# Optimization experiments

Measured on AMD Instinct MI355X. Metric: run time of the kernel, lower is better.

The kernel has to match this reference:

```python
import jax, jax.numpy as jnp
import numpy as np
import itertools

SEQ, NF, K, SD, NB, NC, NOBJ = 8, 4, 3, 256, 512, 174, 10
BELTA, SUB, BATCH = 0.1, 10, 256
SCALES = list(range(NF, 0, -1))  # [4, 3, 2, 1]
D = (K + 1) * SD                 # per-frame fused feature dim = 1024


def _adjust_scales(seq_ind, is_test):
    # mirrors adjust_scale_train / adjust_scale_test
    scale_max = NF * 2
    if seq_ind < scale_max:
        return SCALES[-seq_ind:] if is_test else SCALES[-min(SUB, seq_ind):]
    return SCALES[:min(SUB, seq_ind) + 1]


def _plan(is_test):
    # Static (non-traced) relation-index plan: for each seq_ind, the set of
    # arithmetic-progression frame combinations selected by select_idx().
    plan = []
    for seq_ind in range(1, SEQ + 1):
        entries = []
        for scale in _adjust_scales(seq_ind, is_test):
            k = min(scale, seq_ind)
            division = seq_ind // scale
            sel = [r for r in itertools.combinations(range(seq_ind), k)
                   if np.all(np.diff(np.asarray(r)) == division)]
            if sel:
                entries.append((scale, np.asarray(sel, dtype=np.int32)))
        plan.append(entries)
    return plan


def _temporal_variation(init_input):
    # VLAD-style soft residuals. Source runs kmeans (non-deterministic,
    # numpy/detached); we use deterministic centers = first K points per clip
    # and reproduce the exact downstream math, including the (buggy but
    # faithful) scalar spectral-norm soft assignment shared by all points.
    x = init_input.reshape(-1, SEQ, NOBJ, SD)              # (B, S, O, d)
    flat = x.reshape(x.shape[0], SEQ * NOBJ, SD)           # (B, N, d)
    centers = flat[:, :K, :]                               # (B, K, d)
    diff = flat[:, None, :, :] - centers[:, :, None, :]    # (B, K, N, d)
    sig = jnp.linalg.svd(diff, compute_uv=False)[..., 0]   # matrix 2-norm per (b, k)
    w = jax.nn.softmax(-BELTA * sig ** 2, axis=-1)         # (B, K), same for every point
    # S[b,t,k,:] = sum_o w[b,k] * (x[b,t,o,:] - c[b,k,:])
    var = w[:, None, :, None] * (x.sum(axis=2)[:, :, None, :] - NOBJ * centers[:, None, :, :])
    return jax.lax.stop_gradient(var)  # source detaches via .detach().numpy()


def _fusion(x, w1, b1, w2, b2):
    # Sequential(ReLU, Linear, ReLU, Linear)
    h = jnp.maximum(jax.nn.relu(x) @ w1 + b1, 0.0)
    return h @ w2 + b2


def _forward(graph_out, init_input, params, is_test):
    B = graph_out.shape[0]
    var = _temporal_variation(init_input)                      # (B, S, K, d)
    new_input = jnp.concatenate([var.reshape(B, SEQ, K * SD), graph_out], axis=2)  # (B, S, D)
    rows = []
    for entries in _plan(bool(is_test)):
        acc = jnp.zeros((B, NC), graph_out.dtype)
        for scale, rel in entries:
            # batched gather of all sampled relations at once: (B, R, scale, D)
            g = new_input[:, rel, :].reshape(B, rel.shape[0], scale * D)
            acc = acc + _fusion(g, *params[scale]).sum(axis=1)
        rows.append(acc)
    return jnp.stack(rows, axis=1).reshape(B * SEQ, NC)


def setup_inputs():
    key = jax.random.key(0)
    ks = jax.random.split(key, 2 + 2 * len(SCALES))
    inp = {
        "graph_out": jax.random.normal(ks[0], (BATCH, SEQ, SD), jnp.float32),
        "init_input": jax.random.normal(ks[1], (BATCH * SEQ, NOBJ, SD), jnp.float32),
        "is_test": 0,
    }
    for i, s in enumerate(SCALES):
        inp[f"w1_{s}"] = jax.random.normal(ks[2 + 2 * i], (s * D, NB), jnp.float32) * 0.02
        inp[f"b1_{s}"] = jnp.zeros((NB,), jnp.float32)
        inp[f"w2_{s}"] = jax.random.normal(ks[3 + 2 * i], (NB, NC), jnp.float32) * 0.02
        inp[f"b2_{s}"] = jnp.zeros((NC,), jnp.float32)
    return inp


def reference(graph_out, init_input, is_test, w1_4, b1_4, w2_4, b2_4, w1_3, b1_3, w2_3, b2_3, w1_2, b1_2, w2_2, b2_2, w1_1, b1_1, w2_1, b2_1):
    params = {4: (w1_4, b1_4, w2_4, b2_4), 3: (w1_3, b1_3, w2_3, b2_3),
              2: (w1_2, b1_2, w2_2, b2_2), 1: (w1_1, b1_1, w2_1, b2_1)}
    return _forward(graph_out, init_input, params, is_test)
```

## Files before the change

### kernel.cpp

```cpp
#include <hip/hip_runtime.h>
#include <math.h>
#include <stdint.h>


typedef __attribute__((ext_vector_type(8))) short short8v;
typedef __attribute__((ext_vector_type(4))) short short4v;
typedef __attribute__((ext_vector_type(4))) float f32x4;

__device__ __forceinline__ short f2bf(float f) {
  uint32_t u = __float_as_uint(f);
  u += 0x7fffu + ((u >> 16) & 1u);
  return (short)(u >> 16);
}
__device__ __forceinline__ float bf2f(short s) {
  return __uint_as_float(((uint32_t)(uint16_t)s) << 16);
}
__device__ __forceinline__ void gload16(const void* g, void* l) {
  __builtin_amdgcn_global_load_lds(
      (const __attribute__((address_space(1))) void*)g,
      (__attribute__((address_space(3))) void*)l, 16, 0, 0);
}

__device__ const int8_t ROWS4[12][5] = {
  {3, 0,1,2,3},
  {4, 0,1,2,3},{4, 1,2,3,4},
  {5, 0,1,2,3},{5, 1,2,3,4},{5, 2,3,4,5},
  {6, 0,1,2,3},{6, 1,2,3,4},{6, 2,3,4,5},{6, 3,4,5,6},
  {7, 0,2,4,6},{7, 1,3,5,7},
};
__device__ const int8_t ROWS3[15][4] = {
  {2, 0,1,2},
  {3, 0,1,2},{3, 1,2,3},
  {4, 0,1,2},{4, 1,2,3},{4, 2,3,4},
  {5, 0,2,4},{5, 1,3,5},
  {6, 0,2,4},{6, 1,3,5},{6, 2,4,6},
  {7, 0,2,4},{7, 1,3,5},{7, 2,4,6},{7, 3,5,7},
};
__device__ const int8_t ROWS2[19][3] = {
  {1, 0,1},
  {2, 0,1},{2, 1,2},
  {3, 0,2},{3, 1,3},
  {4, 0,2},{4, 1,3},{4, 2,4},
  {5, 0,3},{5, 1,4},{5, 2,5},
  {6, 0,3},{6, 1,4},{6, 2,5},{6, 3,6},
  {7, 0,4},{7, 1,5},{7, 2,6},{7, 3,7},
};
__device__ const int8_t ROWS1[36][2] = {
  {0,0},
  {1,0},{1,1},
  {2,0},{2,1},{2,2},
  {3,0},{3,1},{3,2},{3,3},
  {4,0},{4,1},{4,2},{4,3},{4,4},
  {5,0},{5,1},{5,2},{5,3},{5,4},{5,5},
  {6,0},{6,1},{6,2},{6,3},{6,4},{6,5},{6,6},
  {7,0},{7,1},{7,2},{7,3},{7,4},{7,5},{7,6},{7,7},
};
__device__ const float CNT[8][4] = {
  {0,0,0,1},{0,0,1,2},{0,1,2,3},{1,2,2,4},
  {2,3,3,5},{3,2,3,6},{4,3,4,7},{2,4,4,8},
};

__device__ const int SL_LO[10]  = {0,1,2,3, 0,1,2, 0,1, 0};
__device__ const int SL_LEN[10] = {4,4,4,5, 4,5,6, 4,7, 8};
__device__ const int SL_PB[10]  = {0,4,8,12,17,21,26,32,36,43};
__device__ const int SL_MT[10]  = {0,8,16,24,34,42,52,64,72,86};

#define GV_FH    0
#define GV_FL    40960
#define GV_S     81920
#define GV_XSUM  109440
#define GV_VK    117632
#define GV_SCAL  118656
#define GV_SZ    118704

__global__ __launch_bounds__(256) void gram_var(
    const float* __restrict__ init, const float* __restrict__ graph,
    short* __restrict__ Rbuf)
{
  __shared__ __align__(16) char smem[GV_SZ];
  short* Fh  = (short*)(smem + GV_FH);
  short* Fl  = (short*)(smem + GV_FL);
  float* Sm  = (float*)(smem + GV_S);
  float* xsm = (float*)(smem + GV_XSUM);
  float* vkb = (float*)(smem + GV_VK);
  float* scal= (float*)(smem + GV_SCAL);

  const int tid = threadIdx.x, lane = tid & 63, w = tid >> 6;
  const int b = blockIdx.x;
  const float* fb = init + (size_t)b * 80 * 256;

  {
    const int t = tid >> 5, kq0 = tid & 31;
#pragma unroll
    for (int h = 0; h < 2; ++h) {
      const int cq = kq0 + h * 32;
      const float* src = fb + (size_t)(t * 10) * 256 + cq * 4;
      f32x4 sum = (f32x4){0.f, 0.f, 0.f, 0.f};
#pragma unroll
      for (int o = 0; o < 10; ++o) {
        f32x4 v = *(const f32x4*)(src + (size_t)o * 256);
        int r = t * 10 + o;
        int byte8 = r * 512 + ((cq * 8) ^ ((r & 7) << 4));
        short4v hv, lv;
#pragma unroll
        for (int e = 0; e < 4; ++e) {
          short hx = f2bf(v[e]);
          hv[e] = hx;
          lv[e] = f2bf(v[e] - bf2f(hx));
        }
        *(short4v*)((char*)Fh + byte8) = hv;
        *(short4v*)((char*)Fl + byte8) = lv;
        sum += v;
      }
      *(f32x4*)(xsm + t * 256 + cq * 4) = sum;
    }
  }
  __syncthreads();

  int ti_[7], tj_[7];
#pragma unroll
  for (int q = 0; q < 7; ++q) {
    int tt = w + q * 4;
    int t5 = (tt < 25) ? tt : 0;
    ti_[q] = t5 / 5; tj_[q] = t5 % 5;
  }
  f32x4 acc[7];
#pragma unroll
  for (int q = 0; q < 7; ++q) acc[q] = (f32x4){0.f, 0.f, 0.f, 0.f};

#pragma unroll
  for (int ks = 0; ks < 8; ++ks) {
    const int koff = ks * 64 + (lane >> 4) * 16;
#pragma unroll
    for (int q = 0; q < 7; ++q) {
      const int tt = w + q * 4;
      if (tt < 25) {
        int ra = ti_[q] * 16 + (lane & 15);
        int rb = tj_[q] * 16 + (lane & 15);
        int ba = ra * 512 + (koff ^ ((ra & 7) << 4));
        int bb = rb * 512 + (koff ^ ((rb & 7) << 4));
        short8v ah = *(const short8v*)((char*)Fh + ba);
        short8v al = *(const short8v*)((char*)Fl + ba);
        short8v bh = *(const short8v*)((char*)Fh + bb);
        short8v bl = *(const short8v*)((char*)Fl + bb);
        acc[q] = __builtin_amdgcn_mfma_f32_16x16x32_bf16(ah, bh, acc[q], 0, 0, 0);
        acc[q] = __builtin_amdgcn_mfma_f32_16x16x32_bf16(ah, bl, acc[q], 0, 0, 0);
        acc[q] = __builtin_amdgcn_mfma_f32_16x16x32_bf16(al, bh, acc[q], 0, 0, 0);
      }
    }
  }
#pragma unroll
  for (int q = 0; q < 7; ++q) {
    const int tt = w + q * 4;
    if (tt < 25) {
      int row0 = ti_[q] * 16 + (lane >> 4) * 4;
      int col = tj_[q] * 16 + (lane & 15);
#pragma unroll
      for (int r = 0; r < 4; ++r) Sm[(row0 + r) * 86 + col] = acc[q][r];
    }
  }
  __syncthreads();

  if (w < 3) {
    const int k = w;
    float* vk = vkb + k * 84;
    const bool has2 = (lane < 16);
    const int r0 = lane, r1 = 64 + lane;
    const float S0k = Sm[r0 * 86 + k];
    const float S1k = has2 ? Sm[r1 * 86 + k] : 0.f;
    const float Skl = Sm[k * 86 + r0];
    const float Skh = has2 ? Sm[k * 86 + r1] : 0.f;
    const float Skk = Sm[k * 86 + k];
    const float* Sr0 = Sm + r0 * 86;
    const float* Sr1 = Sm + r1 * 86;

    float v0 = 1.f, v1 = 1.f;
    vk[r0] = 1.f;
    if (has2) vk[r1] = 1.f;

    float u0f = 0.f, u1f = 0.f;
    for (int it = 0; it < 5; ++it) {
      float u0 = 0.f, u1 = 0.f;
#pragma unroll
      for (int q = 0; q < 40; ++q) {
        float2 vv = *(const float2*)(vk + q * 2);
        float2 a0 = *(const float2*)(Sr0 + q * 2);
        u0 += a0.x * vv.x + a0.y * vv.y;
        if (has2) {
          float2 a1 = *(const float2*)(Sr1 + q * 2);
          u1 += a1.x * vv.x + a1.y * vv.y;
        }
      }
      float sg = v0 + (has2 ? v1 : 0.f);
      float tu = Skl * v0 + (has2 ? Skh * v1 : 0.f);
#pragma unroll
      for (int m = 32; m >= 1; m >>= 1) {
        sg += __shfl_xor(sg, m);
        tu += __shfl_xor(tu, m);
      }
      float un0 = u0 - S0k * sg - tu + Skk * sg;
      float un1 = u1 - S1k * sg - tu + Skk * sg;
      if (it < 4) {
        v0 = un0 * 6.103515625e-05f;
        v1 = un1 * 6.103515625e-05f;
        vk[r0] = v0;
        if (has2) vk[r1] = v1;
      } else {
        u0f = un0; u1f = un1;
      }
    }
    float a = u0f * v0 + (has2 ? u1f * v1 : 0.f);
    float bq = v0 * v0 + (has2 ? v1 * v1 : 0.f);
#pragma unroll
    for (int m = 32; m >= 1; m >>= 1) {
      a += __shfl_xor(a, m);
      bq += __shfl_xor(bq, m);
    }
    if (lane == 0) scal[9 + k] = a / bq;
  }
  __syncthreads();
  if (tid == 0) {
    float L0 = -0.1f * scal[9], L1 = -0.1f * scal[10], L2 = -0.1f * scal[11];
    float m = fmaxf(L0, fmaxf(L1, L2));
    float e0 = expf(L0 - m), e1 = expf(L1 - m), e2 = expf(L2 - m);
    float inv = 1.0f / (e0 + e1 + e2);
    scal[6] = e0 * inv; scal[7] = e1 * inv; scal[8] = e2 * inv;
  }
  __syncthreads();

  {
    const float w0 = scal[6], w1 = scal[7], w2 = scal[8];
    const int d0 = (tid & 63) * 4;
#pragma unroll
    for (int p = 0; p < 2; ++p) {
      const int t = p * 4 + (tid >> 6);
      f32x4 xs = *(const f32x4*)(xsm + t * 256 + d0);
      f32x4 c0 = *(const f32x4*)(fb + 0 * 256 + d0);
      f32x4 c1 = *(const f32x4*)(fb + 1 * 256 + d0);
      f32x4 c2 = *(const f32x4*)(fb + 2 * 256 + d0);
      f32x4 go = *(const f32x4*)(graph + (size_t)(b * 8 + t) * 256 + d0);
      size_t rb = ((size_t)(b * 8 + t)) * 1024;
      short4v s0, s1, s2, s3;
#pragma unroll
      for (int q = 0; q < 4; ++q) {
        float xq = xs[q];
        s0[q] = f2bf(fmaxf(w0 * (xq - 10.f * c0[q]), 0.f));
        s1[q] = f2bf(fmaxf(w1 * (xq - 10.f * c1[q]), 0.f));
        s2[q] = f2bf(fmaxf(w2 * (xq - 10.f * c2[q]), 0.f));
        s3[q] = f2bf(fmaxf(go[q], 0.f));
      }
      *(short4v*)&Rbuf[rb + 0 + d0]   = s0;
      *(short4v*)&Rbuf[rb + 256 + d0] = s1;
      *(short4v*)&Rbuf[rb + 512 + d0] = s2;
      *(short4v*)&Rbuf[rb + 768 + d0] = s3;
    }
  }
}

__global__ __launch_bounds__(512) void prep_weights(
    const float* __restrict__ w1_4, const float* __restrict__ w1_3,
    const float* __restrict__ w1_2, const float* __restrict__ w1_1,
    const float* __restrict__ w2a, const float* __restrict__ w2b,
    const float* __restrict__ w2c, const float* __restrict__ w2d,
    short* __restrict__ W1T, short* __restrict__ W2T)
{
  __shared__ float sh[64 * 65];
  const int blk = blockIdx.x, tid = threadIdx.x;
  if (blk < 1280) {
    const int slice = blk >> 7, rem = blk & 127;
    const int k0 = (rem & 15) * 64, c0 = (rem >> 4) * 64;
    const float* W1; int j;
    if (slice < 4)      { W1 = w1_4; j = slice; }
    else if (slice < 7) { W1 = w1_3; j = slice - 4; }
    else if (slice < 9) { W1 = w1_2; j = slice - 7; }
    else                { W1 = w1_1; j = 0; }
#pragma unroll
    for (int q = tid; q < 1024; q += 512) {
      int r = q >> 4, cq = (q & 15) * 4;
      f32x4 v = *(const f32x4*)(W1 + (size_t)(j * 1024 + k0 + r) * 512 + c0 + cq);
      sh[r * 65 + cq + 0] = v.x; sh[r * 65 + cq + 1] = v.y;
      sh[r * 65 + cq + 2] = v.z; sh[r * 65 + cq + 3] = v.w;
    }
    __syncthreads();
#pragma unroll
    for (int q = tid; q < 1024; q += 512) {
      int cc = q >> 4, kq = (q & 15) * 4;
      short4v sv;
#pragma unroll
      for (int m = 0; m < 4; ++m) sv[m] = f2bf(sh[(kq + m) * 65 + cc]);
      *(short4v*)&W1T[(size_t)(slice * 512 + c0 + cc) * 1024 + k0 + kq] = sv;
    }
  } else {
    int idx = (blk - 1280) * 2048 + tid * 4;
    int col = idx >> 11, kg = idx & 2047;
    int si = kg >> 9, kr = kg & 511;
    const float* w = (si == 0) ? w2a : (si == 1) ? w2b : (si == 2) ? w2c : w2d;
    short4v sv;
#pragma unroll
    for (int q = 0; q < 4; ++q)
      sv[q] = (col < 174) ? f2bf(w[(size_t)(kr + q) * 174 + col]) : (short)0;
    *(short4v*)&W2T[idx] = sv;
  }
}

__global__ __launch_bounds__(256) void p_mfma(
    const short* __restrict__ A, const short* __restrict__ W1T,
    short* __restrict__ P)
{
  __shared__ short As[128 * 32];
  __shared__ short Bs[128 * 32];
  const int id = blockIdx.x;
  const int nid = (id & 7) * 51 + (id >> 3);
  const int ctile = nid & 3;
  const int rest = nid >> 2;
  int sl = 0;
#pragma unroll
  for (int q = 1; q < 10; ++q) if (rest >= SL_MT[q]) sl = q;
  const int mt = rest - SL_MT[sl];
  const int lo = SL_LO[sl];
  const unsigned len = (unsigned)SL_LEN[sl];
  short* Pp = P + (size_t)SL_PB[sl] * 131072;
  const short* Bp = W1T + ((size_t)sl * 512 + (size_t)ctile * 128) * 1024;

  const int tid = threadIdx.x, lane = tid & 63, w = tid >> 6;
  const int wr = w >> 1, wc = w & 1;
  const int rA = w * 16 + (lane >> 2);
  const int kkA = (lane & 3) * 8;
  const unsigned lr0 = (unsigned)(mt * 128 + rA), lr1 = lr0 + 64u;
  const int gr0 = (int)((lr0 / len) * 8u + lo + (lr0 % len));
  const int gr1 = (int)((lr1 / len) * 8u + lo + (lr1 % len));

  f32x4 acc[4][4];
#pragma unroll
  for (int m = 0; m < 4; ++m)
#pragma unroll
    for (int n = 0; n < 4; ++n) acc[m][n] = (f32x4){0.f, 0.f, 0.f, 0.f};

  for (int k0 = 0; k0 < 1024; k0 += 32) {
    __syncthreads();
    gload16(A + (size_t)gr0 * 1024 + k0 + kkA, As + w * 512);
    gload16(A + (size_t)gr1 * 1024 + k0 + kkA, As + 2048 + w * 512);
    gload16(Bp + (size_t)rA * 1024 + k0 + kkA, Bs + w * 512);
    gload16(Bp + (size_t)(64 + rA) * 1024 + k0 + kkA, Bs + 2048 + w * 512);
    __syncthreads();
    short8v a[4], bv[4];
#pragma unroll
    for (int m = 0; m < 4; ++m)
      a[m] = *(const short8v*)(As + (wr * 64 + m * 16 + (lane & 15)) * 32 + (lane >> 4) * 8);
#pragma unroll
    for (int n = 0; n < 4; ++n)
      bv[n] = *(const short8v*)(Bs + (wc * 64 + n * 16 + (lane & 15)) * 32 + (lane >> 4) * 8);
#pragma unroll
    for (int m = 0; m < 4; ++m)
#pragma unroll
      for (int n = 0; n < 4; ++n)
        acc[m][n] = __builtin_amdgcn_mfma_f32_16x16x32_bf16(a[m], bv[n], acc[m][n], 0, 0, 0);
  }

#pragma unroll
  for (int m = 0; m < 4; ++m) {
    int lrow = mt * 128 + wr * 64 + m * 16 + (lane >> 4) * 4;
#pragma unroll
    for (int n = 0; n < 4; ++n) {
      int col = ctile * 128 + wc * 64 + n * 16 + (lane & 15);
#pragma unroll
      for (int r = 0; r < 4; ++r)
        Pp[(size_t)(lrow + r) * 512 + col] = f2bf(acc[m][n][r]);
    }
  }
}

__global__ __launch_bounds__(256) void hsum_all(
    const short* __restrict__ P,
    const float* __restrict__ b1a, const float* __restrict__ b1b,
    const float* __restrict__ b1c, const float* __restrict__ b1d,
    short* __restrict__ Hsum)
{
  const int tid = threadIdx.x;
  const int row = blockIdx.x * 2 + (tid >> 7);
  const int t = row & 7;
  const size_t bq = (size_t)(row >> 3);
  const int c0 = (tid & 127) * 4;

  {
    const int pb[4] = {0, 4 * 131072, 8 * 131072, 12 * 131072};
    const int lo[4] = {0, 1, 2, 3};
    const int ln[4] = {4, 4, 4, 5};
    f32x4 bb = *(const f32x4*)(b1a + c0);
    f32x4 a = (f32x4){0.f, 0.f, 0.f, 0.f};
    for (int r = 0; r < 12; ++r) {
      if (ROWS4[r][0] != t) continue;
      f32x4 h = bb;
#pragma unroll
      for (int jj = 0; jj < 4; ++jj) {
        const short4v pv = *(const short4v*)(P + pb[jj] +
            (bq * ln[jj] + (ROWS4[r][1 + jj] - lo[jj])) * 512 + c0);
#pragma unroll
        for (int e = 0; e < 4; ++e) h[e] += bf2f(pv[e]);
      }
#pragma unroll
      for (int e = 0; e < 4; ++e) a[e] += fmaxf(h[e], 0.f);
    }
    short4v sv;
#pragma unroll
    for (int e = 0; e < 4; ++e) sv[e] = f2bf(a[e]);
    *(short4v*)&Hsum[(size_t)row * 2048 + c0] = sv;
  }
  {
    const int pb[3] = {17 * 131072, 21 * 131072, 26 * 131072};
    const int lo[3] = {0, 1, 2};
    const int ln[3] = {4, 5, 6};
    f32x4 bb = *(const f32x4*)(b1b + c0);
    f32x4 a = (f32x4){0.f, 0.f, 0.f, 0.f};
    for (int r = 0; r < 15; ++r) {
      if (ROWS3[r][0] != t) continue;
      f32x4 h = bb;
#pragma unroll
      for (int jj = 0; jj < 3; ++jj) {
        const short4v pv = *(const short4v*)(P + pb[jj] +
            (bq * ln[jj] + (ROWS3[r][1 + jj] - lo[jj])) * 512 + c0);
#pragma unroll
        for (int e = 0; e < 4; ++e) h[e] += bf2f(pv[e]);
      }
#pragma unroll
      for (int e = 0; e < 4; ++e) a[e] += fmaxf(h[e], 0.f);
    }
    short4v sv;
#pragma unroll
    for (int e = 0; e < 4; ++e) sv[e] = f2bf(a[e]);
    *(short4v*)&Hsum[(size_t)row * 2048 + 512 + c0] = sv;
  }
  {
    const int pb[2] = {32 * 131072, 36 * 131072};
    const int lo[2] = {0, 1};
    const int ln[2] = {4, 7};
    f32x4 bb = *(const f32x4*)(b1c + c0);
    f32x4 a = (f32x4){0.f, 0.f, 0.f, 0.f};
    for (int r = 0; r < 19; ++r) {
      if (ROWS2[r][0] != t) continue;
      f32x4 h = bb;
#pragma unroll
      for (int jj = 0; jj < 2; ++jj) {
        const short4v pv = *(const short4v*)(P + pb[jj] +
            (bq * ln[jj] + (ROWS2[r][1 + jj] - lo[jj])) * 512 + c0);
#pragma unroll
        for (int e = 0; e < 4; ++e) h[e] += bf2f(pv[e]);
      }
#pragma unroll
      for (int e = 0; e < 4; ++e) a[e] += fmaxf(h[e], 0.f);
    }
    short4v sv;
#pragma unroll
    for (int e = 0; e < 4; ++e) sv[e] = f2bf(a[e]);
    *(short4v*)&Hsum[(size_t)row * 2048 + 1024 + c0] = sv;
  }
  {
    f32x4 bb = *(const f32x4*)(b1d + c0);
    f32x4 a = (f32x4){0.f, 0.f, 0.f, 0.f};
    for (int r = 0; r < 36; ++r) {
      if (ROWS1[r][0] != t) continue;
      const short4v pv = *(const short4v*)(P + 43 * 131072 +
          (bq * 8 + ROWS1[r][1]) * 512 + c0);
#pragma unroll
      for (int e = 0; e < 4; ++e) a[e] += fmaxf(bb[e] + bf2f(pv[e]), 0.f);
    }
    short4v sv;
#pragma unroll
    for (int e = 0; e < 4; ++e) sv[e] = f2bf(a[e]);
    *(short4v*)&Hsum[(size_t)row * 2048 + 1536 + c0] = sv;
  }
}

__global__ __launch_bounds__(256) void out_split(
    const short* __restrict__ H, const short* __restrict__ W2T,
    float* __restrict__ partial)
{
  __shared__ short As[128 * 32];
  __shared__ short Bs[64 * 32];
  const int tid = threadIdx.x, lane = tid & 63, w = tid >> 6;
  const int wr = w >> 1, wc = w & 1;
  const int rowBase = blockIdx.y * 128, colBase = blockIdx.x * 64;
  const int kBase = blockIdx.z * 512;
  const int rA = w * 16 + (lane >> 2);
  const int kkA = (lane & 3) * 8;

  f32x4 acc[4][2];
#pragma unroll
  for (int m = 0; m < 4; ++m)
#pragma unroll
    for (int n = 0; n < 2; ++n) acc[m][n] = (f32x4){0.f, 0.f, 0.f, 0.f};

  for (int k0 = 0; k0 < 512; k0 += 32) {
    const int kg = kBase + k0;
    __syncthreads();
    gload16(H + (size_t)(rowBase + rA) * 2048 + kg + kkA, As + w * 512);
    gload16(H + (size_t)(rowBase + 64 + rA) * 2048 + kg + kkA, As + 2048 + w * 512);
    gload16(W2T + (size_t)(colBase + rA) * 2048 + kg + kkA, Bs + w * 512);
    __syncthreads();
    short8v a[4], bv[2];
#pragma unroll
    for (int m = 0; m < 4; ++m)
      a[m] = *(const short8v*)(As + (wr * 64 + m * 16 + (lane & 15)) * 32 + (lane >> 4) * 8);
#pragma unroll
    for (int n = 0; n < 2; ++n)
      bv[n] = *(const short8v*)(Bs + (wc * 32 + n * 16 + (lane & 15)) * 32 + (lane >> 4) * 8);
#pragma unroll
    for (int m = 0; m < 4; ++m)
#pragma unroll
      for (int n = 0; n < 2; ++n)
        acc[m][n] = __builtin_amdgcn_mfma_f32_16x16x32_bf16(a[m], bv[n], acc[m][n], 0, 0, 0);
  }

  float* pz = partial + (size_t)blockIdx.z * 2048 * 192;
#pragma unroll
  for (int n = 0; n < 2; ++n) {
    int col = colBase + wc * 32 + n * 16 + (lane & 15);
#pragma unroll
    for (int m = 0; m < 4; ++m) {
      int row0 = rowBase + wr * 64 + m * 16 + (lane >> 4) * 4;
#pragma unroll
      for (int r = 0; r < 4; ++r)
        pz[(size_t)(row0 + r) * 192 + col] = acc[m][n][r];
    }
  }
}

__global__ __launch_bounds__(256) void out_reduce(
    const float* __restrict__ partial,
    const float* __restrict__ b2a, const float* __restrict__ b2b,
    const float* __restrict__ b2c, const float* __restrict__ b2d,
    float* __restrict__ out)
{
  const int row = blockIdx.x, col = threadIdx.x;
  if (col >= 174) return;
  const size_t o = (size_t)row * 192 + col;
  float s = partial[o] + partial[o + (size_t)2048 * 192]
          + partial[o + (size_t)4096 * 192] + partial[o + (size_t)6144 * 192];
  int tt = row & 7;
  float bias = CNT[tt][0] * b2a[col] + CNT[tt][1] * b2b[col]
             + CNT[tt][2] * b2c[col] + CNT[tt][3] * b2d[col];
  out[(size_t)row * 174 + col] = s + bias;
}

extern "C" void kernel_launch(void* const* d_in, const int* in_sizes, int n_in,
                              void* d_out, int out_size, void* d_ws, size_t ws_size,
                              hipStream_t stream) {
  const float* graph = (const float*)d_in[0];
  const float* init  = (const float*)d_in[1];
  const float* w1[4] = {(const float*)d_in[3],  (const float*)d_in[7],
                        (const float*)d_in[11], (const float*)d_in[15]};
  const float* b1[4] = {(const float*)d_in[4],  (const float*)d_in[8],
                        (const float*)d_in[12], (const float*)d_in[16]};
  const float* w2[4] = {(const float*)d_in[5],  (const float*)d_in[9],
                        (const float*)d_in[13], (const float*)d_in[17]};
  const float* b2[4] = {(const float*)d_in[6],  (const float*)d_in[10],
                        (const float*)d_in[14], (const float*)d_in[18]};
  float* out = (float*)d_out;

  char* ws = (char*)d_ws;
  short* Rbf  = (short*)(ws + 0);
  short* W1T  = (short*)(ws + ((size_t)4  << 20));
  short* P    = (short*)(ws + ((size_t)14 << 20));
  short* W2T  = (short*)(ws + ((size_t)34 << 20));
  short* Hsum = (short*)(ws + 0);
  float* Part = (float*)(ws + ((size_t)8 << 20));

  gram_var<<<256, 256, 0, stream>>>(init, graph, Rbf);

  prep_weights<<<1472, 512, 0, stream>>>(w1[0], w1[1], w1[2], w1[3],
                                         w2[0], w2[1], w2[2], w2[3], W1T, W2T);

  p_mfma<<<408, 256, 0, stream>>>(Rbf, W1T, P);

  hsum_all<<<1024, 256, 0, stream>>>(P, b1[0], b1[1], b1[2], b1[3], Hsum);

  out_split<<<dim3(3, 16, 4), 256, 0, stream>>>(Hsum, W2T, Part);

  out_reduce<<<2048, 256, 0, stream>>>(Part, b2[0], b2[1], b2[2], b2[3], out);
}
```

Baseline: 101.3 us.

## Fuse hidden-sum ReLU reduction with second-layer GEMM through swizzled LDS

Merges hsum_all and out_split into one kernel, hsum_out. Each block builds 32 rows of the ReLU-summed hidden activations for one scale in an XOR-swizzled LDS tile, then multiplies that tile against W2T with MFMA. This removes the global write and re-read of the bf16 Hsum buffer and one kernel launch. In exchange the grid drops to 256 blocks, the hidden-sum phase runs serially over 16 row pairs per block, and W2T fragments are read straight from global memory with no LDS staging.

```diff
diff --git a/kernel.cpp b/kernel.cpp
--- a/kernel.cpp
+++ b/kernel.cpp
@@ -370,162 +370,133 @@
   }
 }
 
-__global__ __launch_bounds__(256) void hsum_all(
-    const short* __restrict__ P,
+__global__ __launch_bounds__(256) void hsum_out(
+    const short* __restrict__ P, const short* __restrict__ W2T,
     const float* __restrict__ b1a, const float* __restrict__ b1b,
     const float* __restrict__ b1c, const float* __restrict__ b1d,
-    short* __restrict__ Hsum)
-{
-  const int tid = threadIdx.x;
-  const int row = blockIdx.x * 2 + (tid >> 7);
-  const int t = row & 7;
-  const size_t bq = (size_t)(row >> 3);
-  const int c0 = (tid & 127) * 4;
-
-  {
-    const int pb[4] = {0, 4 * 131072, 8 * 131072, 12 * 131072};
-    const int lo[4] = {0, 1, 2, 3};
-    const int ln[4] = {4, 4, 4, 5};
-    f32x4 bb = *(const f32x4*)(b1a + c0);
-    f32x4 a = (f32x4){0.f, 0.f, 0.f, 0.f};
-    for (int r = 0; r < 12; ++r) {
-      if (ROWS4[r][0] != t) continue;
-      f32x4 h = bb;
-#pragma unroll
-      for (int jj = 0; jj < 4; ++jj) {
-        const short4v pv = *(const short4v*)(P + pb[jj] +
-            (bq * ln[jj] + (ROWS4[r][1 + jj] - lo[jj])) * 512 + c0);
-#pragma unroll
-        for (int e = 0; e < 4; ++e) h[e] += bf2f(pv[e]);
-      }
-#pragma unroll
-      for (int e = 0; e < 4; ++e) a[e] += fmaxf(h[e], 0.f);
-    }
-    short4v sv;
-#pragma unroll
-    for (int e = 0; e < 4; ++e) sv[e] = f2bf(a[e]);
-    *(short4v*)&Hsum[(size_t)row * 2048 + c0] = sv;
-  }
-  {
-    const int pb[3] = {17 * 131072, 21 * 131072, 26 * 131072};
-    const int lo[3] = {0, 1, 2};
-    const int ln[3] = {4, 5, 6};
-    f32x4 bb = *(const f32x4*)(b1b + c0);
-    f32x4 a = (f32x4){0.f, 0.f, 0.f, 0.f};
-    for (int r = 0; r < 15; ++r) {
-      if (ROWS3[r][0] != t) continue;
-      f32x4 h = bb;
-#pragma unroll
-      for (int jj = 0; jj < 3; ++jj) {
-        const short4v pv = *(const short4v*)(P + pb[jj] +
-            (bq * ln[jj] + (ROWS3[r][1 + jj] - lo[jj])) * 512 + c0);
-#pragma unroll
-        for (int e = 0; e < 4; ++e) h[e] += bf2f(pv[e]);
-      }
-#pragma unroll
-      for (int e = 0; e < 4; ++e) a[e] += fmaxf(h[e], 0.f);
-    }
-    short4v sv;
-#pragma unroll
-    for (int e = 0; e < 4; ++e) sv[e] = f2bf(a[e]);
-    *(short4v*)&Hsum[(size_t)row * 2048 + 512 + c0] = sv;
-  }
-  {
-    const int pb[2] = {32 * 131072, 36 * 131072};
-    const int lo[2] = {0, 1};
-    const int ln[2] = {4, 7};
-    f32x4 bb = *(const f32x4*)(b1c + c0);
-    f32x4 a = (f32x4){0.f, 0.f, 0.f, 0.f};
-    for (int r = 0; r < 19; ++r) {
-      if (ROWS2[r][0] != t) continue;
-      f32x4 h = bb;
-#pragma unroll
-      for (int jj = 0; jj < 2; ++jj) {
-        const short4v pv = *(const short4v*)(P + pb[jj] +
-            (bq * ln[jj] + (ROWS2[r][1 + jj] - lo[jj])) * 512 + c0);
-#pragma unroll
-        for (int e = 0; e < 4; ++e) h[e] += bf2f(pv[e]);
-      }
-#pragma unroll
-      for (int e = 0; e < 4; ++e) a[e] += fmaxf(h[e], 0.f);
-    }
-    short4v sv;
-#pragma unroll
-    for (int e = 0; e < 4; ++e) sv[e] = f2bf(a[e]);
-    *(short4v*)&Hsum[(size_t)row * 2048 + 1024 + c0] = sv;
-  }
-  {
-    f32x4 bb = *(const f32x4*)(b1d + c0);
-    f32x4 a = (f32x4){0.f, 0.f, 0.f, 0.f};
-    for (int r = 0; r < 36; ++r) {
-      if (ROWS1[r][0] != t) continue;
-      const short4v pv = *(const short4v*)(P + 43 * 131072 +
-          (bq * 8 + ROWS1[r][1]) * 512 + c0);
-#pragma unroll
-      for (int e = 0; e < 4; ++e) a[e] += fmaxf(bb[e] + bf2f(pv[e]), 0.f);
-    }
-    short4v sv;
-#pragma unroll
-    for (int e = 0; e < 4; ++e) sv[e] = f2bf(a[e]);
-    *(short4v*)&Hsum[(size_t)row * 2048 + 1536 + c0] = sv;
-  }
-}
-
-__global__ __launch_bounds__(256) void out_split(
-    const short* __restrict__ H, const short* __restrict__ W2T,
     float* __restrict__ partial)
 {
-  __shared__ short As[128 * 32];
-  __shared__ short Bs[64 * 32];
-  const int tid = threadIdx.x, lane = tid & 63, w = tid >> 6;
-  const int wr = w >> 1, wc = w & 1;
-  const int rowBase = blockIdx.y * 128, colBase = blockIdx.x * 64;
-  const int kBase = blockIdx.z * 512;
-  const int rA = w * 16 + (lane >> 2);
-  const int kkA = (lane & 3) * 8;
-
-  f32x4 acc[4][2];
-#pragma unroll
-  for (int m = 0; m < 4; ++m)
-#pragma unroll
-    for (int n = 0; n < 2; ++n) acc[m][n] = (f32x4){0.f, 0.f, 0.f, 0.f};
-
-  for (int k0 = 0; k0 < 512; k0 += 32) {
-    const int kg = kBase + k0;
-    __syncthreads();
-    gload16(H + (size_t)(rowBase + rA) * 2048 + kg + kkA, As + w * 512);
-    gload16(H + (size_t)(rowBase + 64 + rA) * 2048 + kg + kkA, As + 2048 + w * 512);
-    gload16(W2T + (size_t)(colBase + rA) * 2048 + kg + kkA, Bs + w * 512);
-    __syncthreads();
-    short8v a[4], bv[2];
-#pragma unroll
-    for (int m = 0; m < 4; ++m)
-      a[m] = *(const short8v*)(As + (wr * 64 + m * 16 + (lane & 15)) * 32 + (lane >> 4) * 8);
-#pragma unroll
-    for (int n = 0; n < 2; ++n)
-      bv[n] = *(const short8v*)(Bs + (wc * 32 + n * 16 + (lane & 15)) * 32 + (lane >> 4) * 8);
-#pragma unroll
-    for (int m = 0; m < 4; ++m)
-#pragma unroll
-      for (int n = 0; n < 2; ++n)
-        acc[m][n] = __builtin_amdgcn_mfma_f32_16x16x32_bf16(a[m], bv[n], acc[m][n], 0, 0, 0);
-  }
-
-  float* pz = partial + (size_t)blockIdx.z * 2048 * 192;
-#pragma unroll
-  for (int n = 0; n < 2; ++n) {
-    int col = colBase + wc * 32 + n * 16 + (lane & 15);
-#pragma unroll
-    for (int m = 0; m < 4; ++m) {
-      int row0 = rowBase + wr * 64 + m * 16 + (lane >> 4) * 4;
+  __shared__ __align__(16) char HsRaw[32 * 1024];
+  const int tid = threadIdx.x;
+  const int z = blockIdx.y;
+  const int R0 = blockIdx.x * 32;
+
+  {
+    const int c0 = (tid & 127) * 4;
+    const int bofs = c0 * 2;
+    for (int rp = 0; rp < 16; ++rp) {
+      const int lr = rp * 2 + (tid >> 7);
+      const int row = R0 + lr;
+      const int t = row & 7;
+      const size_t bq = (size_t)(row >> 3);
+      f32x4 a = (f32x4){0.f, 0.f, 0.f, 0.f};
+
+      if (z == 0) {
+        const int pb[4] = {0, 4 * 131072, 8 * 131072, 12 * 131072};
+        const int lo[4] = {0, 1, 2, 3};
+        const int ln[4] = {4, 4, 4, 5};
+        f32x4 bb = *(const f32x4*)(b1a + c0);
+        for (int r = 0; r < 12; ++r) {
+          if (ROWS4[r][0] != t) continue;
+          f32x4 h = bb;
+#pragma unroll
+          for (int jj = 0; jj < 4; ++jj) {
+            const short4v pv = *(const short4v*)(P + pb[jj] +
+                (bq * ln[jj] + (ROWS4[r][1 + jj] - lo[jj])) * 512 + c0);
+#pragma unroll
+            for (int e = 0; e < 4; ++e) h[e] += bf2f(pv[e]);
+          }
+#pragma unroll
+          for (int e = 0; e < 4; ++e) a[e] += fmaxf(h[e], 0.f);
+        }
+      } else if (z == 1) {
+        const int pb[3] = {17 * 131072, 21 * 131072, 26 * 131072};
+        const int lo[3] = {0, 1, 2};
+        const int ln[3] = {4, 5, 6};
+        f32x4 bb = *(const f32x4*)(b1b + c0);
+        for (int r = 0; r < 15; ++r) {
+          if (ROWS3[r][0] != t) continue;
+          f32x4 h = bb;
+#pragma unroll
+          for (int jj = 0; jj < 3; ++jj) {
+            const short4v pv = *(const short4v*)(P + pb[jj] +
+                (bq * ln[jj] + (ROWS3[r][1 + jj] - lo[jj])) * 512 + c0);
+#pragma unroll
+            for (int e = 0; e < 4; ++e) h[e] += bf2f(pv[e]);
+          }
+#pragma unroll
+          for (int e = 0; e < 4; ++e) a[e] += fmaxf(h[e], 0.f);
+        }
+      } else if (z == 2) {
+        const int pb[2] = {32 * 131072, 36 * 131072};
+        const int lo[2] = {0, 1};
+        const int ln[2] = {4, 7};
+        f32x4 bb = *(const f32x4*)(b1c + c0);
+        for (int r = 0; r < 19; ++r) {
+          if (ROWS2[r][0] != t) continue;
+          f32x4 h = bb;
+#pragma unroll
+          for (int jj = 0; jj < 2; ++jj) {
+            const short4v pv = *(const short4v*)(P + pb[jj] +
+                (bq * ln[jj] + (ROWS2[r][1 + jj] - lo[jj])) * 512 + c0);
+#pragma unroll
+            for (int e = 0; e < 4; ++e) h[e] += bf2f(pv[e]);
+          }
+#pragma unroll
+          for (int e = 0; e < 4; ++e) a[e] += fmaxf(h[e], 0.f);
+        }
+      } else {
+        f32x4 bb = *(const f32x4*)(b1d + c0);
+        for (int r = 0; r < 36; ++r) {
+          if (ROWS1[r][0] != t) continue;
+          const short4v pv = *(const short4v*)(P + 43 * 131072 +
+              (bq * 8 + ROWS1[r][1]) * 512 + c0);
+#pragma unroll
+          for (int e = 0; e < 4; ++e) a[e] += fmaxf(bb[e] + bf2f(pv[e]), 0.f);
+        }
+      }
+      short4v sv;
+#pragma unroll
+      for (int e = 0; e < 4; ++e) sv[e] = f2bf(a[e]);
+      *(short4v*)(HsRaw + lr * 1024 + (bofs ^ ((lr & 7) << 4))) = sv;
+    }
+  }
+  __syncthreads();
+
+  {
+    const int lane = tid & 63, w = tid >> 6;
+    const int wr = w >> 1, wc = w & 1;
+    f32x4 acc[6];
+#pragma unroll
+    for (int n = 0; n < 6; ++n) acc[n] = (f32x4){0.f, 0.f, 0.f, 0.f};
+
+    const int lrA = wr * 16 + (lane & 15);
+    const short* w2base = W2T + (size_t)z * 512 + (lane >> 4) * 8;
+
+    for (int ks = 0; ks < 16; ++ks) {
+      const int koff = ks * 64 + (lane >> 4) * 16;
+      short8v a = *(const short8v*)(HsRaw + lrA * 1024 + (koff ^ ((lrA & 7) << 4)));
+#pragma unroll
+      for (int n = 0; n < 6; ++n) {
+        int col = wc * 96 + n * 16 + (lane & 15);
+        short8v bv = *(const short8v*)(w2base + (size_t)col * 2048 + ks * 32);
+        acc[n] = __builtin_amdgcn_mfma_f32_16x16x32_bf16(a, bv, acc[n], 0, 0, 0);
+      }
+    }
+
+    float* pz = partial + (size_t)z * 2048 * 192;
+#pragma unroll
+    for (int n = 0; n < 6; ++n) {
+      int col = wc * 96 + n * 16 + (lane & 15);
+      int row0 = R0 + wr * 16 + (lane >> 4) * 4;
 #pragma unroll
       for (int r = 0; r < 4; ++r)
-        pz[(size_t)(row0 + r) * 192 + col] = acc[m][n][r];
-    }
-  }
-}
-
-__global__ __launch_bounds__(256) void out_reduce(
+        pz[(size_t)(row0 + r) * 192 + col] = acc[n][r];
+    }
+  }
+}
+
+__global__ __launch_bounds__(192) void out_reduce(
     const float* __restrict__ partial,
     const float* __restrict__ b2a, const float* __restrict__ b2b,
     const float* __restrict__ b2c, const float* __restrict__ b2d,
@@ -561,9 +532,8 @@
   short* Rbf  = (short*)(ws + 0);
   short* W1T  = (short*)(ws + ((size_t)4  << 20));
   short* P    = (short*)(ws + ((size_t)14 << 20));
+  float* Part = (float*)(ws + ((size_t)27 << 20));
   short* W2T  = (short*)(ws + ((size_t)34 << 20));
-  short* Hsum = (short*)(ws + 0);
-  float* Part = (float*)(ws + ((size_t)8 << 20));
 
   gram_var<<<256, 256, 0, stream>>>(init, graph, Rbf);
 
@@ -572,9 +542,7 @@
 
   p_mfma<<<408, 256, 0, stream>>>(Rbf, W1T, P);
 
-  hsum_all<<<1024, 256, 0, stream>>>(P, b1[0], b1[1], b1[2], b1[3], Hsum);
-
-  out_split<<<dim3(3, 16, 4), 256, 0, stream>>>(Hsum, W2T, Part);
-
-  out_reduce<<<2048, 256, 0, stream>>>(Part, b2[0], b2[1], b2[2], b2[3], out);
-}
+  hsum_out<<<dim3(64, 4), 256, 0, stream>>>(P, W2T, b1[0], b1[1], b1[2], b1[3], Part);
+
+  out_reduce<<<2048, 192, 0, stream>>>(Part, b2[0], b2[1], b2[2], b2[3], out);
+}
```

New measurement: 140.9 us. 39.2% more time.
